# Performance work log

Measured on AMD Instinct MI355X. Metric: run time of the kernel, lower is better.

Reference implementation:

```python
import jax, jax.numpy as jnp
import numpy as np

N = 100000          # nodes
E = 1200000         # edges
IN_DIM = 128
HID = 64
NUM_CLASSES = 5
NUM_GRAPHS = 128


def setup_inputs() -> dict:
    key = jax.random.key(0)
    ks = jax.random.split(key, 12)
    x = jax.random.normal(ks[0], (N, IN_DIM), dtype=jnp.float32)
    edge_index = jax.random.randint(ks[1], (2, E), 0, N, dtype=jnp.int64)
    batch = jnp.sort(jax.random.randint(ks[2], (N,), 0, NUM_GRAPHS, dtype=jnp.int64))
    def glorot(k, shape):
        lim = np.sqrt(6.0 / (shape[0] + shape[1]))
        return jax.random.uniform(k, shape, jnp.float32, -lim, lim)
    W1 = glorot(ks[3], (IN_DIM, HID)); b1 = jnp.zeros((HID,), jnp.float32)
    W2 = glorot(ks[4], (HID, HID));    b2 = jnp.zeros((HID,), jnp.float32)
    W3 = glorot(ks[5], (HID, HID));    b3 = jnp.zeros((HID,), jnp.float32)
    Wc = glorot(ks[6], (HID, NUM_CLASSES)); bc = jnp.zeros((NUM_CLASSES,), jnp.float32)
    return {"x": x, "edge_index": edge_index, "batch": batch,
            "W1": W1, "b1": b1, "W2": W2, "b2": b2, "W3": W3, "b3": b3,
            "Wc": Wc, "bc": bc}


def _gcn_norm(edge_index, n_nodes):
    # PyG GCNConv: add self-loops, symmetric normalization D^-1/2 (A+I) D^-1/2
    loop = jnp.arange(n_nodes, dtype=edge_index.dtype)
    src = jnp.concatenate([edge_index[0], loop])  # [E+N]
    dst = jnp.concatenate([edge_index[1], loop])
    deg = jax.ops.segment_sum(jnp.ones_like(dst, dtype=jnp.float32), dst,
                              num_segments=n_nodes)
    dinv = jnp.where(deg > 0, jax.lax.rsqrt(deg), 0.0)
    norm = dinv[src] * dinv[dst]                   # [E+N]
    return src, dst, norm


def _gcn_conv(x, src, dst, norm, W, b, n_nodes):
    h = x @ W                                      # [N, out]
    msg = h[src] * norm[:, None]                   # gather + scale
    agg = jax.ops.segment_sum(msg, dst, num_segments=n_nodes)  # scatter-add
    return agg + b


def reference(x, edge_index, batch, W1, b1, W2, b2, W3, b3, Wc, bc):
    src, dst, norm = _gcn_norm(edge_index, N)
    h = jax.nn.relu(_gcn_conv(x, src, dst, norm, W1, b1, N))
    h = jax.nn.relu(_gcn_conv(h, src, dst, norm, W2, b2, N))
    h = jax.nn.relu(_gcn_conv(h, src, dst, norm, W3, b3, N))
    # global_mean_pool over batch ids
    sums = jax.ops.segment_sum(h, batch, num_segments=NUM_GRAPHS)
    counts = jax.ops.segment_sum(jnp.ones((N,), jnp.float32), batch,
                                 num_segments=NUM_GRAPHS)
    pooled = sums / jnp.maximum(counts, 1.0)[:, None]  # [G, HID]
    return pooled @ Wc + bc                             # [G, num_classes]
```

## Files before the change

kernel.cpp:

```cpp
#include <hip/hip_runtime.h>
#include <hip/hip_bf16.h>

#define NN 100000
#define NE 1200000
#define IND 128
#define HID 64
#define NC 5
#define NG 128
#define NB 391
#define GB 1172
#define G1 3125

static __device__ __forceinline__ float bf2f(unsigned short u) {
    union { unsigned int i; float f; } x;
    x.i = (unsigned int)u << 16;
    return x.f;
}
static __device__ __forceinline__ unsigned short f2bf(float f) {
    union { float f; unsigned int i; } x;
    x.f = f;
    unsigned int r = (x.i + 0x7fffu + ((x.i >> 16) & 1u)) >> 16;
    return (unsigned short)r;
}

__global__ __launch_bounds__(256) void k_hist(const int* __restrict__ dst, int* __restrict__ cnt,
                                              int* __restrict__ rank) {
    int e = blockIdx.x * 256 + threadIdx.x;
    if (e < NE) rank[e] = atomicAdd(&cnt[dst[e]], 1);
}

__global__ __launch_bounds__(256) void k_scan1(const int* __restrict__ cnt, int* __restrict__ exc,
                                               int* __restrict__ bsum, float* __restrict__ dinv) {
    __shared__ int lds[256];
    int tid = threadIdx.x;
    int i = blockIdx.x * 256 + tid;
    int v = (i < NN) ? cnt[i] : 0;
    lds[tid] = v;
    __syncthreads();
    for (int off = 1; off < 256; off <<= 1) {
        int t = (tid >= off) ? lds[tid - off] : 0;
        __syncthreads();
        lds[tid] += t;
        __syncthreads();
    }
    if (i < NN) {
        exc[i] = lds[tid] - v;
        dinv[i] = rsqrtf((float)v + 1.0f);
    }
    if (tid == 255) bsum[blockIdx.x] = lds[255];
}

__global__ __launch_bounds__(256) void k_scan23(const int* __restrict__ exc, const int* __restrict__ bsum,
                                                int* __restrict__ row_ptr) {
    __shared__ int lds[256];
    int tid = threadIdx.x;
    int me = blockIdx.x;
    int v = 0;
    if (tid < me) v = bsum[tid];
    if (tid + 256 < me) v += bsum[tid + 256];
    lds[tid] = v;
    __syncthreads();
    for (int off = 128; off > 0; off >>= 1) {
        if (tid < off) lds[tid] += lds[tid + off];
        __syncthreads();
    }
    int base = lds[0];
    int i = me * 256 + tid;
    if (i < NN) row_ptr[i] = exc[i] + base;
    if (i == 0) row_ptr[NN] = NE;
}

__global__ __launch_bounds__(256) void k_fused1(
    const float* __restrict__ X, const float* __restrict__ W,
    const float* __restrict__ dinv, unsigned short* __restrict__ out_bf,
    const int* __restrict__ src, const int* __restrict__ dst,
    const int* __restrict__ row_ptr, const int* __restrict__ rank,
    int* __restrict__ src_sorted,
    const int* __restrict__ batch, int* __restrict__ start)
{
    __shared__ float lds[IND * HID + 32 * IND];
    int tid = threadIdx.x;

    if (blockIdx.x < GB) {
        int t = blockIdx.x * 256 + tid;
        const int T = GB * 256;
#pragma unroll
        for (int u = 0; u < 4; ++u) {
            int e = t + u * T;
            if (e < NE) src_sorted[row_ptr[dst[e]] + rank[e]] = src[e];
        }
        return;
    }
    if (blockIdx.x >= GB + G1) {
        int i = (blockIdx.x - GB - G1) * 256 + tid;
        if (i >= NN) return;
        int b = batch[i];
        if (i == 0) {
            for (int g = 0; g <= b; ++g) start[g] = 0;
        } else {
            int p = batch[i - 1];
            for (int g = p + 1; g <= b; ++g) start[g] = i;
        }
        if (i == NN - 1) {
            for (int g = b + 1; g <= NG; ++g) start[g] = NN;
        }
        return;
    }

    float* Wl = lds;
    float* xl = lds + IND * HID;
    int n0 = (blockIdx.x - GB) * 32;
    int c = tid & 31;
    int s = tid >> 5;

    {
        const float4* Wg = (const float4*)W;
        float4* Wl4 = (float4*)Wl;
#pragma unroll
        for (int i = 0; i < IND * 16 / 256; ++i) Wl4[i * 256 + tid] = Wg[i * 256 + tid];
    }
    {
        const float4* Xg = (const float4*)X;
        float4* xl4 = (float4*)xl;
        const float4 z = {0.f, 0.f, 0.f, 0.f};
#pragma unroll
        for (int i = 0; i < 32 * IND / 4 / 256; ++i) {
            int idx = i * 256 + tid;
            int node = n0 + idx / (IND / 4);
            xl4[idx] = (node < NN) ? Xg[(size_t)n0 * (IND / 4) + idx] : z;
        }
    }
    __syncthreads();

    float acc[4][2];
#pragma unroll
    for (int r = 0; r < 4; ++r) { acc[r][0] = 0.f; acc[r][1] = 0.f; }

#pragma unroll 4
    for (int k0 = 0; k0 < IND; k0 += 4) {
        float4 xv[4];
#pragma unroll
        for (int r = 0; r < 4; ++r) xv[r] = *(const float4*)&xl[(s * 4 + r) * IND + k0];
#pragma unroll
        for (int kk = 0; kk < 4; ++kk) {
            float w0 = Wl[(k0 + kk) * HID + c];
            float w1 = Wl[(k0 + kk) * HID + c + 32];
#pragma unroll
            for (int r = 0; r < 4; ++r) {
                float xe = (kk == 0) ? xv[r].x : (kk == 1) ? xv[r].y : (kk == 2) ? xv[r].z : xv[r].w;
                acc[r][0] = fmaf(xe, w0, acc[r][0]);
                acc[r][1] = fmaf(xe, w1, acc[r][1]);
            }
        }
    }

#pragma unroll
    for (int r = 0; r < 4; ++r) {
        int n = n0 + s * 4 + r;
        if (n < NN) {
            float dn = dinv[n];
            out_bf[n * HID + c]      = f2bf(acc[r][0] * dn);
            out_bf[n * HID + c + 32] = f2bf(acc[r][1] * dn);
        }
    }
}

__global__ __launch_bounds__(256) void k_aggregate(const unsigned short* __restrict__ hW,
                                                   const int* __restrict__ srcs,
                                                   const int* __restrict__ row_ptr,
                                                   const float* __restrict__ dinv,
                                                   const float* __restrict__ b,
                                                   unsigned short* __restrict__ outb) {
    const unsigned int* __restrict__ hW4 = (const unsigned int*)hW;
    int tid = threadIdx.x;
    int lane = tid & 63;
    int half = lane >> 5;
    int l = lane & 31;
    int n = blockIdx.x * 4 + (tid >> 6);

    unsigned int su = hW4[(size_t)n * 32 + l];
    float acc0 = half ? 0.f : bf2f((unsigned short)(su & 0xffff));
    float acc1 = half ? 0.f : bf2f((unsigned short)(su >> 16));

    int e = row_ptr[n];
    int end = row_ptr[n + 1];

    for (; e + 7 < end; e += 8) {
        int s0 = srcs[e],     s1 = srcs[e + 1], s2 = srcs[e + 2], s3 = srcs[e + 3];
        int s4 = srcs[e + 4], s5 = srcs[e + 5], s6 = srcs[e + 6], s7 = srcs[e + 7];
        int sa = half ? s1 : s0;
        int sb = half ? s3 : s2;
        int sc = half ? s5 : s4;
        int sd = half ? s7 : s6;
        unsigned int ua = hW4[(size_t)sa * 32 + l];
        unsigned int ub = hW4[(size_t)sb * 32 + l];
        unsigned int uc = hW4[(size_t)sc * 32 + l];
        unsigned int ud = hW4[(size_t)sd * 32 + l];
        acc0 += (bf2f((unsigned short)(ua & 0xffff)) + bf2f((unsigned short)(ub & 0xffff)))
              + (bf2f((unsigned short)(uc & 0xffff)) + bf2f((unsigned short)(ud & 0xffff)));
        acc1 += (bf2f((unsigned short)(ua >> 16)) + bf2f((unsigned short)(ub >> 16)))
              + (bf2f((unsigned short)(uc >> 16)) + bf2f((unsigned short)(ud >> 16)));
    }
    if (e + 3 < end) {
        int s0 = srcs[e], s1 = srcs[e + 1], s2 = srcs[e + 2], s3 = srcs[e + 3];
        int sa = half ? s1 : s0;
        int sb = half ? s3 : s2;
        unsigned int ua = hW4[(size_t)sa * 32 + l];
        unsigned int ub = hW4[(size_t)sb * 32 + l];
        acc0 += bf2f((unsigned short)(ua & 0xffff)) + bf2f((unsigned short)(ub & 0xffff));
        acc1 += bf2f((unsigned short)(ua >> 16)) + bf2f((unsigned short)(ub >> 16));
        e += 4;
    }
    if (e + 1 < end) {
        int s0 = srcs[e], s1 = srcs[e + 1];
        int sa = half ? s1 : s0;
        unsigned int ua = hW4[(size_t)sa * 32 + l];
        acc0 += bf2f((unsigned short)(ua & 0xffff));
        acc1 += bf2f((unsigned short)(ua >> 16));
        e += 2;
    }
    if (e < end && half == 0) {
        int s0 = srcs[e];
        unsigned int ua = hW4[(size_t)s0 * 32 + l];
        acc0 += bf2f((unsigned short)(ua & 0xffff));
        acc1 += bf2f((unsigned short)(ua >> 16));
    }

    acc0 += __shfl_xor(acc0, 32, 64);
    acc1 += __shfl_xor(acc1, 32, 64);

    if (half == 0) {
        float dn = dinv[n];
        float v0 = fmaxf(fmaf(dn, acc0, b[2 * l]), 0.0f);
        float v1 = fmaxf(fmaf(dn, acc1, b[2 * l + 1]), 0.0f);
        unsigned int p = (unsigned int)f2bf(v0) | ((unsigned int)f2bf(v1) << 16);
        ((unsigned int*)outb)[(size_t)n * 32 + l] = p;
    }
}

__global__ __launch_bounds__(256) void k_gemm_bf(const unsigned short* __restrict__ X,
                                                 const float* __restrict__ W,
                                                 const float* __restrict__ dinv,
                                                 unsigned short* __restrict__ outb) {
    __shared__ float Wl[HID * HID];
    __shared__ float xl[64 * HID];
    int tid = threadIdx.x;
    int n0 = blockIdx.x * 64;

    {
        const float4* Wg = (const float4*)W;
        float4* Wl4 = (float4*)Wl;
#pragma unroll
        for (int i = 0; i < HID * HID / 4 / 256; ++i) Wl4[i * 256 + tid] = Wg[i * 256 + tid];
    }
    {
        const uint4* Xg = (const uint4*)X;
#pragma unroll
        for (int i = 0; i < 2; ++i) {
            int idx = i * 256 + tid;
            int ln = idx >> 3;
            int k0 = (idx & 7) * 8;
            int node = n0 + ln;
            float f[8];
            if (node < NN) {
                uint4 u = Xg[(size_t)n0 * 8 + idx];
                f[0] = bf2f((unsigned short)(u.x & 0xffff));
                f[1] = bf2f((unsigned short)(u.x >> 16));
                f[2] = bf2f((unsigned short)(u.y & 0xffff));
                f[3] = bf2f((unsigned short)(u.y >> 16));
                f[4] = bf2f((unsigned short)(u.z & 0xffff));
                f[5] = bf2f((unsigned short)(u.z >> 16));
                f[6] = bf2f((unsigned short)(u.w & 0xffff));
                f[7] = bf2f((unsigned short)(u.w >> 16));
            } else {
#pragma unroll
                for (int q = 0; q < 8; ++q) f[q] = 0.f;
            }
#pragma unroll
            for (int q = 0; q < 8; ++q) xl[ln * HID + k0 + q] = f[q];
        }
    }
    __syncthreads();

    int c = tid & 31;
    int s = tid >> 5;
    float acc[8][2];
#pragma unroll
    for (int r = 0; r < 8; ++r) { acc[r][0] = 0.f; acc[r][1] = 0.f; }

#pragma unroll 4
    for (int k0 = 0; k0 < HID; k0 += 4) {
        float4 xv[8];
#pragma unroll
        for (int r = 0; r < 8; ++r) xv[r] = *(const float4*)&xl[(s * 8 + r) * HID + k0];
#pragma unroll
        for (int kk = 0; kk < 4; ++kk) {
            float w0 = Wl[(k0 + kk) * HID + c];
            float w1 = Wl[(k0 + kk) * HID + c + 32];
#pragma unroll
            for (int r = 0; r < 8; ++r) {
                float xe = (kk == 0) ? xv[r].x : (kk == 1) ? xv[r].y : (kk == 2) ? xv[r].z : xv[r].w;
                acc[r][0] = fmaf(xe, w0, acc[r][0]);
                acc[r][1] = fmaf(xe, w1, acc[r][1]);
            }
        }
    }

#pragma unroll
    for (int r = 0; r < 8; ++r) {
        int n = n0 + s * 8 + r;
        if (n < NN) {
            float dn = dinv[n];
            outb[n * HID + c]      = f2bf(acc[r][0] * dn);
            outb[n * HID + c + 32] = f2bf(acc[r][1] * dn);
        }
    }
}

__global__ __launch_bounds__(256) void k_pool_head(const unsigned short* __restrict__ h,
                                                   const int* __restrict__ start,
                                                   const float* __restrict__ Wc, const float* __restrict__ bc,
                                                   float* __restrict__ out) {
    __shared__ float part[4][HID];
    int g = blockIdx.x;
    int tid = threadIdx.x;
    int j = tid & 63, w = tid >> 6;
    int beg = start[g], end = start[g + 1];
    float acc = 0.0f;
    for (int n = beg + w; n < end; n += 4) acc += bf2f(h[n * HID + j]);
    part[w][j] = acc;
    __syncthreads();
    if (w == 0) {
        float s = part[0][j] + part[1][j] + part[2][j] + part[3][j];
        float cnt = (float)(end - beg);
        float p = s / fmaxf(cnt, 1.0f);
#pragma unroll
        for (int c = 0; c < NC; ++c) {
            float v = p * Wc[j * NC + c];
            for (int off = 32; off > 0; off >>= 1) v += __shfl_down(v, off);
            if (j == 0) out[g * NC + c] = v + bc[c];
        }
    }
}

extern "C" void kernel_launch(void* const* d_in, const int* in_sizes, int n_in,
                              void* d_out, int out_size, void* d_ws, size_t ws_size,
                              hipStream_t stream) {
    const float* x  = (const float*)d_in[0];
    const int* ei   = (const int*)d_in[1];
    const int* bat  = (const int*)d_in[2];
    const float* W1 = (const float*)d_in[3];
    const float* b1 = (const float*)d_in[4];
    const float* W2 = (const float*)d_in[5];
    const float* b2 = (const float*)d_in[6];
    const float* W3 = (const float*)d_in[7];
    const float* b3 = (const float*)d_in[8];
    const float* Wc = (const float*)d_in[9];
    const float* bc = (const float*)d_in[10];
    float* out = (float*)d_out;

    const int* src = ei;
    const int* dst = ei + NE;

    char* wsb = (char*)d_ws;
    float* dinv         = (float*)wsb;
    int*   row_ptr      = (int*)(wsb + 400000);
    int*   srcs         = (int*)(wsb + 800016);
    unsigned short* hWA = (unsigned short*)(wsb + 5600016);
    unsigned short* hWB = (unsigned short*)(wsb + 18400016);
    int*   cnt          = (int*)(wsb + 31200016);
    int*   exc          = (int*)(wsb + 31600016);
    int*   bsum         = (int*)(wsb + 32000016);
    int*   rank         = (int*)(wsb + 32002064);
    int*   start        = (int*)(wsb + 36802064);

    const int gE = (NE + 255) / 256;

    hipMemsetAsync(cnt, 0, NN * sizeof(int), stream);
    k_hist<<<gE, 256, 0, stream>>>(dst, cnt, rank);
    k_scan1<<<NB, 256, 0, stream>>>(cnt, exc, bsum, dinv);
    k_scan23<<<NB, 256, 0, stream>>>(exc, bsum, row_ptr);

    k_fused1<<<GB + G1 + NB, 256, 0, stream>>>(x, W1, dinv, hWA, src, dst, row_ptr, rank, srcs, bat, start);

    k_aggregate<<<NN / 4, 256, 0, stream>>>(hWA, srcs, row_ptr, dinv, b1, hWB);
    k_gemm_bf<<<(NN + 63) / 64, 256, 0, stream>>>(hWB, W2, dinv, hWA);
    k_aggregate<<<NN / 4, 256, 0, stream>>>(hWA, srcs, row_ptr, dinv, b2, hWB);
    k_gemm_bf<<<(NN + 63) / 64, 256, 0, stream>>>(hWB, W3, dinv, hWA);
    k_aggregate<<<NN / 4, 256, 0, stream>>>(hWA, srcs, row_ptr, dinv, b3, hWB);

    k_pool_head<<<NG, 256, 0, stream>>>(hWB, start, Wc, bc, out);
}
```

Measured before the change: 356.0 us.

## Store transformed node features as FP8 to halve gather traffic in aggregation

The GEMM kernels now write the dinv-scaled transformed features as packed FP8 (two values per 16-bit store) instead of bf16. The aggregation kernel gathers 64-byte rows with 16 lanes per edge and four edges per wavefront, unpacking FP8 with hardware conversion builtins, then reduces across lane groups with shuffles. This targets the memory traffic of the random neighbor gathers, which dominate aggregation. In exchange it adds precision loss from 8-bit storage of intermediate activations, which may approach tolerance limits.

New measurement: 343.6 us. 3.5% less time.

```diff
diff --git a/kernel.cpp b/kernel.cpp
--- a/kernel.cpp
+++ b/kernel.cpp
@@ -11,6 +11,8 @@
 #define GB 1172
 #define G1 3125
 
+typedef float v2f __attribute__((ext_vector_type(2)));
+
 static __device__ __forceinline__ float bf2f(unsigned short u) {
     union { unsigned int i; float f; } x;
     x.i = (unsigned int)u << 16;
@@ -22,6 +24,15 @@
     unsigned int r = (x.i + 0x7fffu + ((x.i >> 16) & 1u)) >> 16;
     return (unsigned short)r;
 }
+static __device__ __forceinline__ unsigned short f2fp8x2(float a, float b) {
+    int p = __builtin_amdgcn_cvt_pk_fp8_f32(a, b, 0, false);
+    return (unsigned short)(p & 0xffff);
+}
+static __device__ __forceinline__ void fp8acc(unsigned int u, float& a0, float& a1, float& a2, float& a3) {
+    v2f lo = __builtin_amdgcn_cvt_pk_f32_fp8(u, false);
+    v2f hi = __builtin_amdgcn_cvt_pk_f32_fp8(u, true);
+    a0 += lo.x; a1 += lo.y; a2 += hi.x; a3 += hi.y;
+}
 
 __global__ __launch_bounds__(256) void k_hist(const int* __restrict__ dst, int* __restrict__ cnt,
                                               int* __restrict__ rank) {
@@ -72,7 +83,7 @@
 
 __global__ __launch_bounds__(256) void k_fused1(
     const float* __restrict__ X, const float* __restrict__ W,
-    const float* __restrict__ dinv, unsigned short* __restrict__ out_bf,
+    const float* __restrict__ dinv, unsigned short* __restrict__ out_f8,
     const int* __restrict__ src, const int* __restrict__ dst,
     const int* __restrict__ row_ptr, const int* __restrict__ rank,
     int* __restrict__ src_sorted,
@@ -143,8 +154,8 @@
         for (int r = 0; r < 4; ++r) xv[r] = *(const float4*)&xl[(s * 4 + r) * IND + k0];
 #pragma unroll
         for (int kk = 0; kk < 4; ++kk) {
-            float w0 = Wl[(k0 + kk) * HID + c];
-            float w1 = Wl[(k0 + kk) * HID + c + 32];
+            float w0 = Wl[(k0 + kk) * HID + 2 * c];
+            float w1 = Wl[(k0 + kk) * HID + 2 * c + 1];
 #pragma unroll
             for (int r = 0; r < 4; ++r) {
                 float xe = (kk == 0) ? xv[r].x : (kk == 1) ? xv[r].y : (kk == 2) ? xv[r].z : xv[r].w;
@@ -159,89 +170,80 @@
         int n = n0 + s * 4 + r;
         if (n < NN) {
             float dn = dinv[n];
-            out_bf[n * HID + c]      = f2bf(acc[r][0] * dn);
-            out_bf[n * HID + c + 32] = f2bf(acc[r][1] * dn);
-        }
-    }
-}
-
-__global__ __launch_bounds__(256) void k_aggregate(const unsigned short* __restrict__ hW,
+            out_f8[(size_t)n * 32 + c] = f2fp8x2(acc[r][0] * dn, acc[r][1] * dn);
+        }
+    }
+}
+
+__global__ __launch_bounds__(256) void k_aggregate(const unsigned int* __restrict__ hW8,
                                                    const int* __restrict__ srcs,
                                                    const int* __restrict__ row_ptr,
                                                    const float* __restrict__ dinv,
                                                    const float* __restrict__ b,
-                                                   unsigned short* __restrict__ outb) {
-    const unsigned int* __restrict__ hW4 = (const unsigned int*)hW;
+                                                   unsigned int* __restrict__ outb) {
     int tid = threadIdx.x;
     int lane = tid & 63;
-    int half = lane >> 5;
-    int l = lane & 31;
+    int grp = lane >> 4;
+    int li = lane & 15;
     int n = blockIdx.x * 4 + (tid >> 6);
 
-    unsigned int su = hW4[(size_t)n * 32 + l];
-    float acc0 = half ? 0.f : bf2f((unsigned short)(su & 0xffff));
-    float acc1 = half ? 0.f : bf2f((unsigned short)(su >> 16));
+    float a0 = 0.f, a1 = 0.f, a2 = 0.f, a3 = 0.f;
+    if (grp == 0) {
+        unsigned int su = hW8[(size_t)n * 16 + li];
+        fp8acc(su, a0, a1, a2, a3);
+    }
 
     int e = row_ptr[n];
     int end = row_ptr[n + 1];
 
     for (; e + 7 < end; e += 8) {
-        int s0 = srcs[e],     s1 = srcs[e + 1], s2 = srcs[e + 2], s3 = srcs[e + 3];
-        int s4 = srcs[e + 4], s5 = srcs[e + 5], s6 = srcs[e + 6], s7 = srcs[e + 7];
-        int sa = half ? s1 : s0;
-        int sb = half ? s3 : s2;
-        int sc = half ? s5 : s4;
-        int sd = half ? s7 : s6;
-        unsigned int ua = hW4[(size_t)sa * 32 + l];
-        unsigned int ub = hW4[(size_t)sb * 32 + l];
-        unsigned int uc = hW4[(size_t)sc * 32 + l];
-        unsigned int ud = hW4[(size_t)sd * 32 + l];
-        acc0 += (bf2f((unsigned short)(ua & 0xffff)) + bf2f((unsigned short)(ub & 0xffff)))
-              + (bf2f((unsigned short)(uc & 0xffff)) + bf2f((unsigned short)(ud & 0xffff)));
-        acc1 += (bf2f((unsigned short)(ua >> 16)) + bf2f((unsigned short)(ub >> 16)))
-              + (bf2f((unsigned short)(uc >> 16)) + bf2f((unsigned short)(ud >> 16)));
+        int sA = srcs[e + grp];
+        int sB = srcs[e + 4 + grp];
+        unsigned int uA = hW8[(size_t)sA * 16 + li];
+        unsigned int uB = hW8[(size_t)sB * 16 + li];
+        fp8acc(uA, a0, a1, a2, a3);
+        fp8acc(uB, a0, a1, a2, a3);
     }
     if (e + 3 < end) {
-        int s0 = srcs[e], s1 = srcs[e + 1], s2 = srcs[e + 2], s3 = srcs[e + 3];
-        int sa = half ? s1 : s0;
-        int sb = half ? s3 : s2;
-        unsigned int ua = hW4[(size_t)sa * 32 + l];
-        unsigned int ub = hW4[(size_t)sb * 32 + l];
-        acc0 += bf2f((unsigned short)(ua & 0xffff)) + bf2f((unsigned short)(ub & 0xffff));
-        acc1 += bf2f((unsigned short)(ua >> 16)) + bf2f((unsigned short)(ub >> 16));
+        int sA = srcs[e + grp];
+        unsigned int uA = hW8[(size_t)sA * 16 + li];
+        fp8acc(uA, a0, a1, a2, a3);
         e += 4;
     }
-    if (e + 1 < end) {
-        int s0 = srcs[e], s1 = srcs[e + 1];
-        int sa = half ? s1 : s0;
-        unsigned int ua = hW4[(size_t)sa * 32 + l];
-        acc0 += bf2f((unsigned short)(ua & 0xffff));
-        acc1 += bf2f((unsigned short)(ua >> 16));
-        e += 2;
-    }
-    if (e < end && half == 0) {
-        int s0 = srcs[e];
-        unsigned int ua = hW4[(size_t)s0 * 32 + l];
-        acc0 += bf2f((unsigned short)(ua & 0xffff));
-        acc1 += bf2f((unsigned short)(ua >> 16));
-    }
-
-    acc0 += __shfl_xor(acc0, 32, 64);
-    acc1 += __shfl_xor(acc1, 32, 64);
-
-    if (half == 0) {
+    int rem = end - e;
+    if (grp < rem) {
+        int sA = srcs[e + grp];
+        unsigned int uA = hW8[(size_t)sA * 16 + li];
+        fp8acc(uA, a0, a1, a2, a3);
+    }
+
+    a0 += __shfl_xor(a0, 16, 64);
+    a1 += __shfl_xor(a1, 16, 64);
+    a2 += __shfl_xor(a2, 16, 64);
+    a3 += __shfl_xor(a3, 16, 64);
+    a0 += __shfl_xor(a0, 32, 64);
+    a1 += __shfl_xor(a1, 32, 64);
+    a2 += __shfl_xor(a2, 32, 64);
+    a3 += __shfl_xor(a3, 32, 64);
+
+    if (lane < 16) {
         float dn = dinv[n];
-        float v0 = fmaxf(fmaf(dn, acc0, b[2 * l]), 0.0f);
-        float v1 = fmaxf(fmaf(dn, acc1, b[2 * l + 1]), 0.0f);
-        unsigned int p = (unsigned int)f2bf(v0) | ((unsigned int)f2bf(v1) << 16);
-        ((unsigned int*)outb)[(size_t)n * 32 + l] = p;
+        float4 bv = ((const float4*)b)[li];
+        float v0 = fmaxf(fmaf(dn, a0, bv.x), 0.0f);
+        float v1 = fmaxf(fmaf(dn, a1, bv.y), 0.0f);
+        float v2 = fmaxf(fmaf(dn, a2, bv.z), 0.0f);
+        float v3 = fmaxf(fmaf(dn, a3, bv.w), 0.0f);
+        uint2 p;
+        p.x = (unsigned int)f2bf(v0) | ((unsigned int)f2bf(v1) << 16);
+        p.y = (unsigned int)f2bf(v2) | ((unsigned int)f2bf(v3) << 16);
+        ((uint2*)outb)[(size_t)n * 16 + li] = p;
     }
 }
 
 __global__ __launch_bounds__(256) void k_gemm_bf(const unsigned short* __restrict__ X,
                                                  const float* __restrict__ W,
                                                  const float* __restrict__ dinv,
-                                                 unsigned short* __restrict__ outb) {
+                                                 unsigned short* __restrict__ out_f8) {
     __shared__ float Wl[HID * HID];
     __shared__ float xl[64 * HID];
     int tid = threadIdx.x;
@@ -295,8 +297,8 @@
         for (int r = 0; r < 8; ++r) xv[r] = *(const float4*)&xl[(s * 8 + r) * HID + k0];
 #pragma unroll
         for (int kk = 0; kk < 4; ++kk) {
-            float w0 = Wl[(k0 + kk) * HID + c];
-            float w1 = Wl[(k0 + kk) * HID + c + 32];
+            float w0 = Wl[(k0 + kk) * HID + 2 * c];
+            float w1 = Wl[(k0 + kk) * HID + 2 * c + 1];
 #pragma unroll
             for (int r = 0; r < 8; ++r) {
                 float xe = (kk == 0) ? xv[r].x : (kk == 1) ? xv[r].y : (kk == 2) ? xv[r].z : xv[r].w;
@@ -311,8 +313,7 @@
         int n = n0 + s * 8 + r;
         if (n < NN) {
             float dn = dinv[n];
-            outb[n * HID + c]      = f2bf(acc[r][0] * dn);
-            outb[n * HID + c + 32] = f2bf(acc[r][1] * dn);
+            out_f8[(size_t)n * 32 + c] = f2fp8x2(acc[r][0] * dn, acc[r][1] * dn);
         }
     }
 }
@@ -366,8 +367,8 @@
     float* dinv         = (float*)wsb;
     int*   row_ptr      = (int*)(wsb + 400000);
     int*   srcs         = (int*)(wsb + 800016);
-    unsigned short* hWA = (unsigned short*)(wsb + 5600016);
-    unsigned short* hWB = (unsigned short*)(wsb + 18400016);
+    unsigned short* hF8 = (unsigned short*)(wsb + 5600016);
+    unsigned short* hBF = (unsigned short*)(wsb + 18400016);
     int*   cnt          = (int*)(wsb + 31200016);
     int*   exc          = (int*)(wsb + 31600016);
     int*   bsum         = (int*)(wsb + 32000016);
@@ -381,13 +382,13 @@
     k_scan1<<<NB, 256, 0, stream>>>(cnt, exc, bsum, dinv);
     k_scan23<<<NB, 256, 0, stream>>>(exc, bsum, row_ptr);
 
-    k_fused1<<<GB + G1 + NB, 256, 0, stream>>>(x, W1, dinv, hWA, src, dst, row_ptr, rank, srcs, bat, start);
-
-    k_aggregate<<<NN / 4, 256, 0, stream>>>(hWA, srcs, row_ptr, dinv, b1, hWB);
-    k_gemm_bf<<<(NN + 63) / 64, 256, 0, stream>>>(hWB, W2, dinv, hWA);
-    k_aggregate<<<NN / 4, 256, 0, stream>>>(hWA, srcs, row_ptr, dinv, b2, hWB);
-    k_gemm_bf<<<(NN + 63) / 64, 256, 0, stream>>>(hWB, W3, dinv, hWA);
-    k_aggregate<<<NN / 4, 256, 0, stream>>>(hWA, srcs, row_ptr, dinv, b3, hWB);
-
-    k_pool_head<<<NG, 256, 0, stream>>>(hWB, start, Wc, bc, out);
-}
+    k_fused1<<<GB + G1 + NB, 256, 0, stream>>>(x, W1, dinv, hF8, src, dst, row_ptr, rank, srcs, bat, start);
+
+    k_aggregate<<<NN / 4, 256, 0, stream>>>((const unsigned int*)hF8, srcs, row_ptr, dinv, b1, (unsigned int*)hBF);
+    k_gemm_bf<<<(NN + 63) / 64, 256, 0, stream>>>(hBF, W2, dinv, hF8);
+    k_aggregate<<<NN / 4, 256, 0, stream>>>((const unsigned int*)hF8, srcs, row_ptr, dinv, b2, (unsigned int*)hBF);
+    k_gemm_bf<<<(NN + 63) / 64, 256, 0, stream>>>(hBF, W3, dinv, hF8);
+    k_aggregate<<<NN / 4, 256, 0, stream>>>((const unsigned int*)hF8, srcs, row_ptr, dinv, b3, (unsigned int*)hBF);
+
+    k_pool_head<<<NG, 256, 0, stream>>>(hBF, start, Wc, bc, out);
+}
```
